# Optimization experiments

Hardware: AMD Instinct MI355X
Metric: run time of the kernel (lower is better)

Reference implementation:

```python
import jax, jax.numpy as jnp
import numpy as np

NUM_EMBEDDINGS = 8192
EMBEDDING_DIM = 256
COMMITMENT_COST = 0.25


def setup_inputs() -> dict:
    key = jax.random.key(0)
    k1, k2 = jax.random.split(key)
    hidden_states = jax.random.normal(k1, (16, EMBEDDING_DIM, 32, 32), dtype=jnp.float32)
    # nn.Embedding init: uniform(-1/K, 1/K)
    emb_weights = jax.random.uniform(
        k2, (NUM_EMBEDDINGS, EMBEDDING_DIM), dtype=jnp.float32,
        minval=-1.0 / NUM_EMBEDDINGS, maxval=1.0 / NUM_EMBEDDINGS)
    return {"hidden_states": hidden_states, "emb_weights": emb_weights}


def reference(hidden_states, emb_weights):
    # (B, C, H, W) -> (B, H, W, C) -> (N, C)
    h = jnp.transpose(hidden_states, (0, 2, 3, 1))
    flat = h.reshape(-1, EMBEDDING_DIM)
    # squared L2 distance to every codebook entry: (N, K)
    distance = (jnp.sum(flat * flat, axis=1, keepdims=True)
                + jnp.sum(emb_weights * emb_weights, axis=1)
                - 2.0 * flat @ emb_weights.T)
    min_encoding_indices = jnp.argmin(distance, axis=1)  # (N,)
    # direct gather (same math as one-hot @ codebook in the original)
    z_q = emb_weights[min_encoding_indices].reshape(h.shape)  # (B, H, W, C)
    # return_loss=True path
    loss = (jnp.mean((jax.lax.stop_gradient(z_q) - h) ** 2)
            + COMMITMENT_COST * jnp.mean((z_q - jax.lax.stop_gradient(h)) ** 2))
    # straight-through estimator
    z_q = h + jax.lax.stop_gradient(z_q - h)
    z_q = jnp.transpose(z_q, (0, 3, 1, 2))  # back to (B, C, H, W)
    min_encoding_indices = min_encoding_indices.reshape(h.shape[0], -1)
    return z_q, min_encoding_indices, loss
```

## Files before the change

kernel.cpp:

```cpp
#include <hip/hip_runtime.h>


#define N_ROWS 16384
#define K_CAND 8192
#define CDIM   256
#define NELEM  4194304

#define SA_FLT   0
#define SK_FLT   16384
#define SL_FLT   49152
#define SQC_FLT  49160
#define SBB_FLT  51208
#define SQ_FLT   59400
#define SFB_FLT  1337352
#define SEB_FLT  3434504
#define QCAP     624

typedef __attribute__((ext_vector_type(8))) short short8;
typedef __attribute__((ext_vector_type(4))) float f32x4;
typedef __attribute__((ext_vector_type(4))) unsigned uint32x4;

__device__ __forceinline__ unsigned short f2bf_rne(float x) {
    unsigned u = __float_as_uint(x);
    return (unsigned short)((u + 0x7fffu + ((u >> 16) & 1u)) >> 16);
}
__device__ __forceinline__ float bf2f(unsigned short u) {
    return __uint_as_float(((unsigned)u) << 16);
}
__device__ __forceinline__ unsigned ordU(float f) {
    unsigned u = __float_as_uint(f);
    return u ^ (((int)u >> 31) | 0x80000000u);
}

__global__ void kA(const float* __restrict__ hs, float* __restrict__ out) {
    float* A = out + SA_FLT;
    unsigned long long* keys = (unsigned long long*)(out + SK_FLT);
    int n = blockIdx.x * 256 + threadIdx.x;
    keys[n] = ~0ull;
    if (n == 0) *(double*)(out + SL_FLT) = 0.0;
    int b = n >> 10, yx = n & 1023;
    const float* base = hs + ((size_t)b << 18) + yx;
    float hsum[2];
    for (int h = 0; h < 2; ++h) {
        float r[8];
        #pragma unroll
        for (int j = 0; j < 8; ++j) {
            float x = base[(size_t)(h * 128 + j) << 10];
            r[j] = __fmul_rn(x, x);
        }
        for (int i = 8; i < 128; i += 8) {
            #pragma unroll
            for (int j = 0; j < 8; ++j) {
                float x = base[(size_t)(h * 128 + i + j) << 10];
                r[j] = __fadd_rn(r[j], __fmul_rn(x, x));
            }
        }
        hsum[h] = __fadd_rn(
            __fadd_rn(__fadd_rn(r[0], r[1]), __fadd_rn(r[2], r[3])),
            __fadd_rn(__fadd_rn(r[4], r[5]), __fadd_rn(r[6], r[7])));
    }
    A[n] = __fadd_rn(hsum[0], hsum[1]);
}

__global__ void kFbf(const float* __restrict__ hs, float* __restrict__ out) {
    unsigned short* fbf = (unsigned short*)(out + SFB_FLT);
    __shared__ float T[64][65];
    int blk = blockIdx.x;
    int b = blk >> 6, cB = (blk >> 4) & 3, yB = blk & 15;
    int t = threadIdx.x;
    int yl = t & 63, ch = t >> 6;
    const float* src = hs + ((size_t)b << 18) + (((size_t)cB * 64) << 10) + yB * 64 + yl;
    #pragma unroll
    for (int i = 0; i < 16; ++i) {
        int c = ch * 16 + i;
        T[c][yl] = src[(size_t)c << 10];
    }
    __syncthreads();
    int yr = t >> 2, cs = (t & 3) * 16;
    short8 v0, v1;
    #pragma unroll
    for (int j = 0; j < 8; ++j) {
        v0[j] = (short)f2bf_rne(2.0f * T[cs + j][yr]);
        v1[j] = (short)f2bf_rne(2.0f * T[cs + 8 + j][yr]);
    }
    unsigned short* dst = fbf + (((size_t)(b * 1024 + yB * 64 + yr)) << 8) + cB * 64 + cs;
    *(short8*)dst = v0;
    *(short8*)(dst + 8) = v1;
}

__global__ void kEbf(const float* __restrict__ emb, float* __restrict__ out) {
    unsigned short* ebf = (unsigned short*)(out + SEB_FLT);
    float* bbfNeg = out + SBB_FLT;
    int cand = blockIdx.x * 64 + threadIdx.x;
    const float* ep = emb + ((size_t)cand << 8);
    unsigned short* dp = ebf + (((size_t)(cand >> 4)) << 12) + (cand & 15) * 8;
    float s = 0.f;
    for (int c0 = 0; c0 < 256; c0 += 8) {
        short8 v;
        #pragma unroll
        for (int j = 0; j < 8; ++j) {
            unsigned short bb = f2bf_rne(ep[c0 + j]);
            v[j] = (short)bb;
            float eh = bf2f(bb);
            s = fmaf(eh, eh, s);
        }
        *(short8*)(dp + (c0 >> 3) * 128) = v;
    }
    bbfNeg[cand] = -s;
}

__global__ __launch_bounds__(256, 3) void kScr(const float* __restrict__ hs,
                                               const float* __restrict__ emb,
                                               float* __restrict__ out) {
    const float* A = out + SA_FLT;
    unsigned* qcount = (unsigned*)(out + SQC_FLT);
    const float* bbfNeg = out + SBB_FLT;
    unsigned* queue = (unsigned*)(out + SQ_FLT);
    const unsigned short* fbf = (const unsigned short*)(out + SFB_FLT);
    const unsigned short* ebf = (const unsigned short*)(out + SEB_FLT);

    __shared__ __align__(16) short As2[16384];
    __shared__ unsigned rowMaxOrd[64];
    __shared__ float margLds[64];
    __shared__ int lqnH[2];

    const int t = threadIdx.x, blk = blockIdx.x;
    const int row0 = (blk >> 2) * 64;
    const int candSplit = (blk & 3) * 2048;
    const int lane = t & 63, wid = t >> 6;
    const int quad = lane >> 4, l15 = lane & 15;
    const int qb0 = (blk >> 2) * 8 + (blk & 3);
    unsigned* qB[2] = { queue + (size_t)qb0 * QCAP,
                        queue + (size_t)(qb0 + 4) * QCAP };

    if (t < 64) {
        rowMaxOrd[t] = 0u;
        margLds[t] = 2.0e-5f * sqrtf(A[row0 + t]) + 4.0e-5f;
    }
    if (t < 2) lqnH[t] = 0;

    {
        const unsigned short* src = fbf + ((size_t)row0 << 8);
        #pragma unroll
        for (int i = 0; i < 8; ++i) {
            int d = i * 256 + t;
            short8 v = *(const short8*)(src + d * 8);
            int r = d >> 5, c32 = d & 31;
            int D = ((r >> 4) << 9) + (c32 << 4) + (r & 15);
            *(short8*)&As2[D << 3] = v;
        }
    }
    __syncthreads();

    f32x4 mgv[4];
    #pragma unroll
    for (int m = 0; m < 4; ++m)
        mgv[m] = *(const f32x4*)&margLds[m * 16 + quad * 4];

    for (int cc = 0; cc < 8; ++cc) {
        const int candW = candSplit + cc * 256 + wid * 64;
        const unsigned short* ebW = ebf + (((size_t)candW) << 8)
                                       + quad * 128 + l15 * 8;
        float bneg[4];
        #pragma unroll
        for (int jc = 0; jc < 4; ++jc)
            bneg[jc] = bbfNeg[candW + jc * 16 + l15];

        f32x4 acc[4][4];
        #pragma unroll
        for (int jc = 0; jc < 4; ++jc)
            #pragma unroll
            for (int m = 0; m < 4; ++m)
                acc[m][jc] = (f32x4){0.f, 0.f, 0.f, 0.f};
        #pragma unroll
        for (int ks = 0; ks < 8; ++ks) {
            short8 bf[4];
            #pragma unroll
            for (int jc = 0; jc < 4; ++jc)
                bf[jc] = *(const short8*)(ebW + jc * 4096 + ks * 512);
            #pragma unroll
            for (int m = 0; m < 4; ++m) {
                short8 af = *(const short8*)&As2[(((m * 8 + ks) << 6) + lane) << 3];
                #pragma unroll
                for (int jc = 0; jc < 4; ++jc)
                    acc[m][jc] = __builtin_amdgcn_mfma_f32_16x16x32_bf16(
                        af, bf[jc], acc[m][jc], 0, 0, 0);
            }
        }
        #pragma unroll
        for (int m = 0; m < 4; ++m) {
            uint32x4 thv = *(const uint32x4*)&rowMaxOrd[m * 16 + quad * 4];
            #pragma unroll
            for (int reg = 0; reg < 4; ++reg) {
                int rl = m * 16 + quad * 4 + reg;
                float x0 = __fadd_rn(acc[m][0][reg], bneg[0]);
                float x1 = __fadd_rn(acc[m][1][reg], bneg[1]);
                float x2 = __fadd_rn(acc[m][2][reg], bneg[2]);
                float x3 = __fadd_rn(acc[m][3][reg], bneg[3]);
                float vmax = fmaxf(fmaxf(x0, x1), fmaxf(x2, x3));
                unsigned th = thv[reg];
                float mg = mgv[m][reg];
                bool hot = ordU(__fadd_rn(vmax, mg)) >= th;
                unsigned long long bal = __ballot(hot);
                if (((bal >> (quad * 16)) & 0xFFFFull) == 0ull) continue;
                float g = vmax;
                g = fmaxf(g, __shfl_xor(g, 1, 16));
                g = fmaxf(g, __shfl_xor(g, 2, 16));
                g = fmaxf(g, __shfl_xor(g, 4, 16));
                g = fmaxf(g, __shfl_xor(g, 8, 16));
                unsigned og = ordU(g);
                if (og > th) { atomicMax(&rowMaxOrd[rl], og); th = og; }
                float xs[4] = {x0, x1, x2, x3};
                #pragma unroll
                for (int jc = 0; jc < 4; ++jc) {
                    if (ordU(__fadd_rn(xs[jc], mg)) >= th) {
                        int slot = atomicAdd(&lqnH[m >> 1], 1);
                        if (slot < QCAP)
                            qB[m >> 1][slot] = ((unsigned)(rl & 31) << 13)
                                             | (unsigned)(candW + jc * 16 + l15);
                    }
                }
            }
        }
    }
    __syncthreads();
    if (t < 2) qcount[qb0 + t * 4] = (unsigned)lqnH[t];
}

__global__ __launch_bounds__(256, 4) void kTailE(const float* __restrict__ hs,
                                                 const float* __restrict__ emb,
                                                 float* __restrict__ out) {
    const float* A = out + SA_FLT;
    unsigned long long* keys = (unsigned long long*)(out + SK_FLT);
    const unsigned* qcount = (const unsigned*)(out + SQC_FLT);
    const unsigned* queue = (const unsigned*)(out + SQ_FLT);

    __shared__ __align__(16) float F[32][264];

    const int t = threadIdx.x, blk = blockIdx.x;
    const int row0 = (blk >> 2) * 32;
    const unsigned* qBlk = queue + (size_t)blk * QCAP;

    int n = (int)qcount[blk];
    if (n == 0) return;

    {
        int yl = t & 31, cq = t >> 5;
        int nrow = row0 + yl;
        int b = nrow >> 10, yx = nrow & 1023;
        const float* src = hs + ((size_t)b << 18) + yx;
        #pragma unroll
        for (int i = 0; i < 32; ++i) {
            int c = i * 8 + cq;
            F[yl][c] = src[(size_t)c << 10];
        }
    }
    __syncthreads();

    if (n > QCAP) {
        int cb = (blk & 3) * 2048;
        for (int p = t; p < 32 * 2048; p += 256) {
            int rl = p >> 11, cand = cb + (p & 2047);
            const float* ep = emb + ((size_t)cand << 8);
            float acc = 0.f;
            #pragma unroll 8
            for (int c0 = 0; c0 < 256; c0 += 4) {
                f32x4 f4 = *(const f32x4*)&F[rl][c0];
                f32x4 e4 = *(const f32x4*)(ep + c0);
                acc = fmaf(f4[0], e4[0], acc);
                acc = fmaf(f4[1], e4[1], acc);
                acc = fmaf(f4[2], e4[2], acc);
                acc = fmaf(f4[3], e4[3], acc);
            }
            int row = row0 + rl;
            float d = __fsub_rn(A[row], __fadd_rn(acc, acc));
            unsigned long long key =
                ((unsigned long long)__float_as_uint(d) << 32) | (unsigned)cand;
            atomicMin(&keys[row], key);
        }
        return;
    }

    for (int i = t; i < n; i += 256) {
        unsigned e = qBlk[i];
        int rl = (int)(e >> 13), cand = (int)(e & 8191u);
        const float* ep = emb + ((size_t)cand << 8);
        float acc = 0.f;
        #pragma unroll 8
        for (int c0 = 0; c0 < 256; c0 += 4) {
            f32x4 f4 = *(const f32x4*)&F[rl][c0];
            f32x4 e4 = *(const f32x4*)(ep + c0);
            acc = fmaf(f4[0], e4[0], acc);
            acc = fmaf(f4[1], e4[1], acc);
            acc = fmaf(f4[2], e4[2], acc);
            acc = fmaf(f4[3], e4[3], acc);
        }
        int row = row0 + rl;
        float d = __fsub_rn(A[row], __fadd_rn(acc, acc));
        unsigned long long key =
            ((unsigned long long)__float_as_uint(d) << 32) | (unsigned)cand;
        atomicMin(&keys[row], key);
    }
}

__global__ void kPost(float* __restrict__ out) {
    const unsigned long long* keys = (const unsigned long long*)(out + SK_FLT);
    double* lossAcc = (double*)(out + SL_FLT);
    __shared__ double sd[256];
    int n = blockIdx.x * 256 + threadIdx.x;
    unsigned long long key = keys[n];
    unsigned idx = (unsigned)(key & 0xffffffffu) & 8191u;
    float d = __uint_as_float((unsigned)(key >> 32));
    out[NELEM + n] = (float)idx;
    sd[threadIdx.x] = (double)d;
    __syncthreads();
    for (int s = 128; s > 0; s >>= 1) {
        if (threadIdx.x < s) sd[threadIdx.x] += sd[threadIdx.x + s];
        __syncthreads();
    }
    if (threadIdx.x == 0) atomicAdd(lossAcc, sd[0]);
}

__global__ void kLoss(float* __restrict__ out) {
    if (threadIdx.x == 0) {
        double loss = 1.25 * (*(const double*)(out + SL_FLT)) / (double)NELEM;
        out[NELEM + N_ROWS] = (float)loss;
    }
}

__global__ __launch_bounds__(256) void kZQ(const float* __restrict__ hs,
                                           const float* __restrict__ emb,
                                           float* __restrict__ out) {
    __shared__ float E[64][65];
    __shared__ unsigned idxL[64];

    const int t = threadIdx.x, blk = blockIdx.x;
    const int nt = blk >> 2, ct = blk & 3;
    const int row0 = nt * 64, c0 = ct * 64;
    const int b = row0 >> 10, yx0 = row0 & 1023;

    if (t < 64) idxL[t] = (unsigned)out[NELEM + row0 + t] & 8191u;
    __syncthreads();

    {
        int r = t >> 2, j = t & 3;
        const float* ep = emb + ((size_t)idxL[r] << 8) + c0 + j * 16;
        #pragma unroll
        for (int q = 0; q < 4; ++q) {
            f32x4 v = *(const f32x4*)(ep + q * 4);
            #pragma unroll
            for (int i = 0; i < 4; ++i)
                E[j * 16 + q * 4 + i][r] = v[i];
        }
    }
    __syncthreads();

    {
        int yl = t & 63, ch = t >> 6;
        #pragma unroll
        for (int i = 0; i < 16; ++i) {
            int cl = ch * 16 + i;
            size_t o = ((size_t)b << 18) | ((size_t)(c0 + cl) << 10)
                     | (size_t)(yx0 + yl);
            float h = hs[o];
            float e = E[cl][yl];
            out[o] = __fadd_rn(h, __fsub_rn(e, h));
        }
    }
}

extern "C" void kernel_launch(void* const* d_in, const int* in_sizes, int n_in,
                              void* d_out, int out_size, void* d_ws, size_t ws_size,
                              hipStream_t stream) {
    const float* hs  = (const float*)d_in[0];
    const float* emb = (const float*)d_in[1];
    float* out = (float*)d_out;

    kA<<<N_ROWS / 256, 256, 0, stream>>>(hs, out);
    kFbf<<<1024, 256, 0, stream>>>(hs, out);
    kEbf<<<K_CAND / 64, 64, 0, stream>>>(emb, out);
    kScr<<<1024, 256, 0, stream>>>(hs, emb, out);
    kTailE<<<2048, 256, 0, stream>>>(hs, emb, out);
    kPost<<<N_ROWS / 256, 256, 0, stream>>>(out);
    kLoss<<<1, 64, 0, stream>>>(out);
    kZQ<<<1024, 256, 0, stream>>>(hs, emb, out);
}
```

Before: 349.1 us.

## Fuse norm and bf16 prep, swizzle LDS A-tile, merge tail and post kernels

Merges the row-norm kernel and the bf16 transpose kernel into one kernel that reads hidden_states once through a shared tile. It adds an XOR swizzle to the A-operand LDS layout in the scoring kernel to cut bank conflicts on MFMA fragment loads. The tail re-rank kernel now processes all four candidate splits per row block in one block, which reduces the grid and reloads F less often. The post/index/loss reduction is folded into the z_q gather kernel using wave shuffles. Fewer launches and less redundant global traffic come at the cost of less parallelism in the tail kernel.

```diff
diff --git a/kernel.cpp b/kernel.cpp
--- a/kernel.cpp
+++ b/kernel.cpp
@@ -32,60 +32,64 @@
     return u ^ (((int)u >> 31) | 0x80000000u);
 }
 
-__global__ void kA(const float* __restrict__ hs, float* __restrict__ out) {
+__global__ __launch_bounds__(256) void kAF(const float* __restrict__ hs,
+                                           float* __restrict__ out) {
     float* A = out + SA_FLT;
     unsigned long long* keys = (unsigned long long*)(out + SK_FLT);
-    int n = blockIdx.x * 256 + threadIdx.x;
-    keys[n] = ~0ull;
-    if (n == 0) *(double*)(out + SL_FLT) = 0.0;
-    int b = n >> 10, yx = n & 1023;
-    const float* base = hs + ((size_t)b << 18) + yx;
-    float hsum[2];
-    for (int h = 0; h < 2; ++h) {
+    unsigned short* fbf = (unsigned short*)(out + SFB_FLT);
+    __shared__ float T[256][33];
+
+    const int t = threadIdx.x, blk = blockIdx.x;
+    const int b = blk >> 5, yB = blk & 31;
+    const int row0 = b * 1024 + yB * 32;
+    if (blk == 0 && t == 0) *(double*)(out + SL_FLT) = 0.0;
+    if (t < 32) keys[row0 + t] = ~0ull;
+
+    {
+        int yl = t & 31, ch = t >> 5;
+        const float* src = hs + ((size_t)b << 18) + yB * 32 + yl;
+        #pragma unroll
+        for (int i = 0; i < 32; ++i) {
+            int c = i * 8 + ch;
+            T[c][yl] = src[(size_t)c << 10];
+        }
+    }
+    __syncthreads();
+
+    if (t < 64) {
+        int yl = t & 31, h = t >> 5;
         float r[8];
         #pragma unroll
         for (int j = 0; j < 8; ++j) {
-            float x = base[(size_t)(h * 128 + j) << 10];
+            float x = T[h * 128 + j][yl];
             r[j] = __fmul_rn(x, x);
         }
         for (int i = 8; i < 128; i += 8) {
             #pragma unroll
             for (int j = 0; j < 8; ++j) {
-                float x = base[(size_t)(h * 128 + i + j) << 10];
+                float x = T[h * 128 + i + j][yl];
                 r[j] = __fadd_rn(r[j], __fmul_rn(x, x));
             }
         }
-        hsum[h] = __fadd_rn(
+        float hsum = __fadd_rn(
             __fadd_rn(__fadd_rn(r[0], r[1]), __fadd_rn(r[2], r[3])),
             __fadd_rn(__fadd_rn(r[4], r[5]), __fadd_rn(r[6], r[7])));
-    }
-    A[n] = __fadd_rn(hsum[0], hsum[1]);
-}
-
-__global__ void kFbf(const float* __restrict__ hs, float* __restrict__ out) {
-    unsigned short* fbf = (unsigned short*)(out + SFB_FLT);
-    __shared__ float T[64][65];
-    int blk = blockIdx.x;
-    int b = blk >> 6, cB = (blk >> 4) & 3, yB = blk & 15;
-    int t = threadIdx.x;
-    int yl = t & 63, ch = t >> 6;
-    const float* src = hs + ((size_t)b << 18) + (((size_t)cB * 64) << 10) + yB * 64 + yl;
-    #pragma unroll
-    for (int i = 0; i < 16; ++i) {
-        int c = ch * 16 + i;
-        T[c][yl] = src[(size_t)c << 10];
-    }
-    __syncthreads();
-    int yr = t >> 2, cs = (t & 3) * 16;
-    short8 v0, v1;
-    #pragma unroll
-    for (int j = 0; j < 8; ++j) {
-        v0[j] = (short)f2bf_rne(2.0f * T[cs + j][yr]);
-        v1[j] = (short)f2bf_rne(2.0f * T[cs + 8 + j][yr]);
-    }
-    unsigned short* dst = fbf + (((size_t)(b * 1024 + yB * 64 + yr)) << 8) + cB * 64 + cs;
-    *(short8*)dst = v0;
-    *(short8*)(dst + 8) = v1;
+        float other = __shfl_down(hsum, 32);
+        if (h == 0) A[row0 + yl] = __fadd_rn(hsum, other);
+    }
+
+    {
+        int yl = t & 31, cq = t >> 5;
+        unsigned short* dst = fbf + (((size_t)(row0 + yl)) << 8) + cq * 32;
+        #pragma unroll
+        for (int v = 0; v < 4; ++v) {
+            short8 w;
+            #pragma unroll
+            for (int j = 0; j < 8; ++j)
+                w[j] = (short)f2bf_rne(2.0f * T[cq * 32 + v * 8 + j][yl]);
+            *(short8*)(dst + v * 8) = w;
+        }
+    }
 }
 
 __global__ void kEbf(const float* __restrict__ emb, float* __restrict__ out) {
@@ -147,10 +151,14 @@
             short8 v = *(const short8*)(src + d * 8);
             int r = d >> 5, c32 = d & 31;
             int D = ((r >> 4) << 9) + (c32 << 4) + (r & 15);
+            D ^= (c32 & 7);
             *(short8*)&As2[D << 3] = v;
         }
     }
     __syncthreads();
+
+    const int off0 = ((quad << 4) + (l15 ^ quad)) << 3;
+    const int off1 = ((quad << 4) + (l15 ^ quad ^ 4)) << 3;
 
     f32x4 mgv[4];
     #pragma unroll
@@ -180,7 +188,8 @@
                 bf[jc] = *(const short8*)(ebW + jc * 4096 + ks * 512);
             #pragma unroll
             for (int m = 0; m < 4; ++m) {
-                short8 af = *(const short8*)&As2[(((m * 8 + ks) << 6) + lane) << 3];
+                short8 af = *(const short8*)&As2[((m * 8 + ks) << 9)
+                                                 + ((ks & 1) ? off1 : off0)];
                 #pragma unroll
                 for (int jc = 0; jc < 4; ++jc)
                     acc[m][jc] = __builtin_amdgcn_mfma_f32_16x16x32_bf16(
@@ -227,7 +236,7 @@
     if (t < 2) qcount[qb0 + t * 4] = (unsigned)lqnH[t];
 }
 
-__global__ __launch_bounds__(256, 4) void kTailE(const float* __restrict__ hs,
+__global__ __launch_bounds__(256, 4) void kTailM(const float* __restrict__ hs,
                                                  const float* __restrict__ emb,
                                                  float* __restrict__ out) {
     const float* A = out + SA_FLT;
@@ -237,12 +246,13 @@
 
     __shared__ __align__(16) float F[32][264];
 
-    const int t = threadIdx.x, blk = blockIdx.x;
-    const int row0 = (blk >> 2) * 32;
-    const unsigned* qBlk = queue + (size_t)blk * QCAP;
-
-    int n = (int)qcount[blk];
-    if (n == 0) return;
+    const int t = threadIdx.x, R = blockIdx.x;
+    const int row0 = R * 32;
+
+    int nq[4];
+    #pragma unroll
+    for (int s = 0; s < 4; ++s) nq[s] = (int)qcount[R * 4 + s];
+    if ((nq[0] | nq[1] | nq[2] | nq[3]) == 0) return;
 
     {
         int yl = t & 31, cq = t >> 5;
@@ -257,10 +267,36 @@
     }
     __syncthreads();
 
-    if (n > QCAP) {
-        int cb = (blk & 3) * 2048;
-        for (int p = t; p < 32 * 2048; p += 256) {
-            int rl = p >> 11, cand = cb + (p & 2047);
+    for (int s = 0; s < 4; ++s) {
+        int n = nq[s];
+        if (n == 0) continue;
+        if (n > QCAP) {
+            int cb = s * 2048;
+            for (int p = t; p < 32 * 2048; p += 256) {
+                int rl = p >> 11, cand = cb + (p & 2047);
+                const float* ep = emb + ((size_t)cand << 8);
+                float acc = 0.f;
+                #pragma unroll 8
+                for (int c0 = 0; c0 < 256; c0 += 4) {
+                    f32x4 f4 = *(const f32x4*)&F[rl][c0];
+                    f32x4 e4 = *(const f32x4*)(ep + c0);
+                    acc = fmaf(f4[0], e4[0], acc);
+                    acc = fmaf(f4[1], e4[1], acc);
+                    acc = fmaf(f4[2], e4[2], acc);
+                    acc = fmaf(f4[3], e4[3], acc);
+                }
+                int row = row0 + rl;
+                float d = __fsub_rn(A[row], __fadd_rn(acc, acc));
+                unsigned long long key =
+                    ((unsigned long long)__float_as_uint(d) << 32) | (unsigned)cand;
+                atomicMin(&keys[row], key);
+            }
+            continue;
+        }
+        const unsigned* qBlk = queue + (size_t)(R * 4 + s) * QCAP;
+        for (int i = t; i < n; i += 256) {
+            unsigned e = qBlk[i];
+            int rl = (int)(e >> 13), cand = (int)(e & 8191u);
             const float* ep = emb + ((size_t)cand << 8);
             float acc = 0.f;
             #pragma unroll 8
@@ -278,59 +314,13 @@
                 ((unsigned long long)__float_as_uint(d) << 32) | (unsigned)cand;
             atomicMin(&keys[row], key);
         }
-        return;
-    }
-
-    for (int i = t; i < n; i += 256) {
-        unsigned e = qBlk[i];
-        int rl = (int)(e >> 13), cand = (int)(e & 8191u);
-        const float* ep = emb + ((size_t)cand << 8);
-        float acc = 0.f;
-        #pragma unroll 8
-        for (int c0 = 0; c0 < 256; c0 += 4) {
-            f32x4 f4 = *(const f32x4*)&F[rl][c0];
-            f32x4 e4 = *(const f32x4*)(ep + c0);
-            acc = fmaf(f4[0], e4[0], acc);
-            acc = fmaf(f4[1], e4[1], acc);
-            acc = fmaf(f4[2], e4[2], acc);
-            acc = fmaf(f4[3], e4[3], acc);
-        }
-        int row = row0 + rl;
-        float d = __fsub_rn(A[row], __fadd_rn(acc, acc));
-        unsigned long long key =
-            ((unsigned long long)__float_as_uint(d) << 32) | (unsigned)cand;
-        atomicMin(&keys[row], key);
-    }
-}
-
-__global__ void kPost(float* __restrict__ out) {
+    }
+}
+
+__global__ __launch_bounds__(256) void kZQf(const float* __restrict__ hs,
+                                            const float* __restrict__ emb,
+                                            float* __restrict__ out) {
     const unsigned long long* keys = (const unsigned long long*)(out + SK_FLT);
-    double* lossAcc = (double*)(out + SL_FLT);
-    __shared__ double sd[256];
-    int n = blockIdx.x * 256 + threadIdx.x;
-    unsigned long long key = keys[n];
-    unsigned idx = (unsigned)(key & 0xffffffffu) & 8191u;
-    float d = __uint_as_float((unsigned)(key >> 32));
-    out[NELEM + n] = (float)idx;
-    sd[threadIdx.x] = (double)d;
-    __syncthreads();
-    for (int s = 128; s > 0; s >>= 1) {
-        if (threadIdx.x < s) sd[threadIdx.x] += sd[threadIdx.x + s];
-        __syncthreads();
-    }
-    if (threadIdx.x == 0) atomicAdd(lossAcc, sd[0]);
-}
-
-__global__ void kLoss(float* __restrict__ out) {
-    if (threadIdx.x == 0) {
-        double loss = 1.25 * (*(const double*)(out + SL_FLT)) / (double)NELEM;
-        out[NELEM + N_ROWS] = (float)loss;
-    }
-}
-
-__global__ __launch_bounds__(256) void kZQ(const float* __restrict__ hs,
-                                           const float* __restrict__ emb,
-                                           float* __restrict__ out) {
     __shared__ float E[64][65];
     __shared__ unsigned idxL[64];
 
@@ -339,7 +329,22 @@
     const int row0 = nt * 64, c0 = ct * 64;
     const int b = row0 >> 10, yx0 = row0 & 1023;
 
-    if (t < 64) idxL[t] = (unsigned)out[NELEM + row0 + t] & 8191u;
+    if (t < 64) {
+        unsigned long long key = keys[row0 + t];
+        unsigned idx = (unsigned)key & 8191u;
+        idxL[t] = idx;
+        if (ct == 0) {
+            out[NELEM + row0 + t] = (float)idx;
+            double d = (double)__uint_as_float((unsigned)(key >> 32));
+            d += __shfl_down(d, 32);
+            d += __shfl_down(d, 16);
+            d += __shfl_down(d, 8);
+            d += __shfl_down(d, 4);
+            d += __shfl_down(d, 2);
+            d += __shfl_down(d, 1);
+            if (t == 0) atomicAdd((double*)(out + SL_FLT), d);
+        }
+    }
     __syncthreads();
 
     {
@@ -369,6 +374,13 @@
     }
 }
 
+__global__ void kLoss(float* __restrict__ out) {
+    if (threadIdx.x == 0) {
+        double loss = 1.25 * (*(const double*)(out + SL_FLT)) / (double)NELEM;
+        out[NELEM + N_ROWS] = (float)loss;
+    }
+}
+
 extern "C" void kernel_launch(void* const* d_in, const int* in_sizes, int n_in,
                               void* d_out, int out_size, void* d_ws, size_t ws_size,
                               hipStream_t stream) {
@@ -376,12 +388,10 @@
     const float* emb = (const float*)d_in[1];
     float* out = (float*)d_out;
 
-    kA<<<N_ROWS / 256, 256, 0, stream>>>(hs, out);
-    kFbf<<<1024, 256, 0, stream>>>(hs, out);
+    kAF<<<512, 256, 0, stream>>>(hs, out);
     kEbf<<<K_CAND / 64, 64, 0, stream>>>(emb, out);
     kScr<<<1024, 256, 0, stream>>>(hs, emb, out);
-    kTailE<<<2048, 256, 0, stream>>>(hs, emb, out);
-    kPost<<<N_ROWS / 256, 256, 0, stream>>>(out);
+    kTailM<<<512, 256, 0, stream>>>(hs, emb, out);
+    kZQf<<<1024, 256, 0, stream>>>(hs, emb, out);
     kLoss<<<1, 64, 0, stream>>>(out);
-    kZQ<<<1024, 256, 0, stream>>>(hs, emb, out);
-}
+}
```

Measured after the change: 302.8 us. 1.15x faster.
